# Kernel tuning notes

Measured on AMD Instinct MI355X. Metric: run time of the kernel, lower is better.

## Reference

```python
import jax, jax.numpy as jnp
import numpy as np

B, N_IN, N_OUT, H = 64, 5023, 5023, 256
EPS = 1e-12  # matches torch F.normalize default eps


def setup_inputs() -> dict:
    key = jax.random.key(0)
    k1, k2, k3, k4 = jax.random.split(key, 4)
    return {
        "x": jax.random.normal(k1, (B, N_IN, 3), dtype=jnp.float32),
        "key_w": jax.random.normal(k2, (N_IN, H), dtype=jnp.float32) * (1.0 / np.sqrt(H)),
        "query_w": jax.random.normal(k3, (H, N_OUT), dtype=jnp.float32) * (1.0 / np.sqrt(H)),
        "value_w": jax.random.normal(k4, (3, 3), dtype=jnp.float32),
    }


def reference(x, key_w, query_w, value_w):
    # v = nn.Linear(3,3,bias=False)(x): x @ W^T        [B, N_in, 3]
    v = jnp.einsum("bnd,ed->bne", x, value_w)
    # score = (key @ query) / sqrt(hidden_dim)          [N_in, N_out]
    scale = jnp.asarray(key_w.shape[-1], x.dtype) ** 0.5
    score = jnp.matmul(key_w, query_w) / scale
    # L1 normalization along dim=1 (F.normalize p=1)
    l1 = jnp.sum(jnp.abs(score), axis=1, keepdims=True)
    score = score / jnp.maximum(l1, EPS)
    # y = score.T @ v (dropout is identity in eval / p=0) [B, N_out, 3]
    return jnp.einsum("io,bid->bod", score, v)
```

## Files before the change

### kernel.cpp

```cpp
#include <hip/hip_runtime.h>
#include <hip/hip_bf16.h>

#define N_IN   5023
#define B_SZ   64
#define H_DIM  256
#define NPAD   5120
#define NBD    192
#define SPLITZ 80
#define OUT_ELEMS (B_SZ * N_IN * 3)

typedef short bf16x8 __attribute__((ext_vector_type(8)));
typedef float f32x4  __attribute__((ext_vector_type(4)));
typedef int   i32x4  __attribute__((ext_vector_type(4)));
typedef int   i32x8  __attribute__((ext_vector_type(8)));

__device__ inline void async_copy16(const void* g, void* l) {
    __builtin_amdgcn_global_load_lds(
        (const __attribute__((address_space(1))) unsigned int*)g,
        (__attribute__((address_space(3))) unsigned int*)l,
        16, 0, 0);
}

__device__ inline unsigned char to_fp8(float v) {
    int p = __builtin_amdgcn_cvt_pk_fp8_f32(v, 0.0f, 0, false);
    return (unsigned char)(p & 0xFF);
}

__global__ void conv_all(const float* __restrict__ kw, const float* __restrict__ qw,
                         unsigned char* __restrict__ k8, short* __restrict__ keyT,
                         unsigned char* __restrict__ q8, short* __restrict__ qtb,
                         float* __restrict__ l1) {
    __shared__ float tile[32][33];
    const int hb = blockIdx.x * 32;
    const int nb = blockIdx.y * 32;
    const int tx = threadIdx.x;
    const int ty = threadIdx.y;
    if (blockIdx.z == 0) {
        for (int j = 0; j < 32; j += 8) {
            int i = nb + ty + j;
            int h = hb + tx;
            float v = (i < N_IN) ? kw[(size_t)i * H_DIM + h] : 0.0f;
            tile[ty + j][tx] = v;
            k8[(size_t)i * H_DIM + h] = to_fp8(v);
        }
        __syncthreads();
        __hip_bfloat16* kt = (__hip_bfloat16*)keyT;
        for (int j = 0; j < 32; j += 8) {
            int h = hb + ty + j;
            int i = nb + tx;
            kt[(size_t)h * NPAD + i] = __float2bfloat16(tile[tx][ty + j]);
        }
        if (blockIdx.x == 0 && ty == 0) l1[nb + tx] = 0.0f;
    } else {
        for (int j = 0; j < 32; j += 8) {
            int h = hb + ty + j;
            int o = nb + tx;
            tile[ty + j][tx] = (o < N_IN) ? qw[(size_t)h * N_IN + o] : 0.0f;
        }
        __syncthreads();
        __hip_bfloat16* qt = (__hip_bfloat16*)qtb;
        for (int j = 0; j < 32; j += 8) {
            int o = nb + ty + j;
            int h = hb + tx;
            float v = tile[tx][ty + j];
            qt[(size_t)o * H_DIM + h] = __float2bfloat16(v * 0.0625f);
            q8[(size_t)o * H_DIM + h] = to_fp8(v);
        }
    }
}

__launch_bounds__(256)
__global__ void gemm_l1(const unsigned char* __restrict__ q8,
                        const unsigned char* __restrict__ k8,
                        float* __restrict__ l1) {
    __shared__ unsigned char As8[128 * 128];
    __shared__ unsigned char Bs8[128 * 128];
    const int bm = blockIdx.x, bn = blockIdx.y;
    const int tid = threadIdx.x, lane = tid & 63, wid = tid >> 6;
    const int wave_m = wid >> 1, wave_n = wid & 1;
    const int r = lane >> 3;
    const int s = lane & 7;
    const int quad = lane >> 4, cit = lane & 15;
    const int xk = cit & 7;

    f32x4 acc[4][4];
    const f32x4 zf = {0.f, 0.f, 0.f, 0.f};
    for (int a = 0; a < 4; ++a)
        for (int b = 0; b < 4; ++b) acc[a][b] = zf;

    const int g0 = (2 * quad) ^ xk;
    const int g1 = (2 * quad + 1) ^ xk;

    for (int kb = 0; kb < H_DIM; kb += 128) {
        __syncthreads();
        const int koff = kb + ((s ^ r) << 4);
        for (int c = 0; c < 4; ++c) {
            int q = wid * 4 + c;
            int row = q * 8 + r;
            async_copy16(q8 + (size_t)(bm * 128 + row) * H_DIM + koff, As8 + q * 1024);
            async_copy16(k8 + (size_t)(bn * 128 + row) * H_DIM + koff, Bs8 + q * 1024);
        }
        __syncthreads();
        i32x8 af[4];
        for (int t = 0; t < 4; ++t) {
            const unsigned char* pa = As8 + (wave_m * 64 + t * 16 + cit) * 128;
            i32x4 lo = *(const i32x4*)(pa + (g0 << 4));
            i32x4 hi = *(const i32x4*)(pa + (g1 << 4));
            af[t] = __builtin_shufflevector(lo, hi, 0, 1, 2, 3, 4, 5, 6, 7);
        }
        for (int tn = 0; tn < 4; ++tn) {
            const unsigned char* pb = Bs8 + (wave_n * 64 + tn * 16 + cit) * 128;
            i32x4 lo = *(const i32x4*)(pb + (g0 << 4));
            i32x4 hi = *(const i32x4*)(pb + (g1 << 4));
            i32x8 bf = __builtin_shufflevector(lo, hi, 0, 1, 2, 3, 4, 5, 6, 7);
            for (int tm = 0; tm < 4; ++tm)
                acc[tm][tn] = __builtin_amdgcn_mfma_scale_f32_16x16x128_f8f6f4(
                    af[tm], bf, acc[tm][tn], 0, 0,
                    0, 0x7F7F7F7F,
                    0, 0x7F7F7F7F);
        }
    }

    for (int tn = 0; tn < 4; ++tn) {
        int ig = bn * 128 + wave_n * 64 + tn * 16 + cit;
        float p = 0.0f;
        for (int tm = 0; tm < 4; ++tm) {
            f32x4 c = acc[tm][tn];
            p += fabsf(c.x) + fabsf(c.y) + fabsf(c.z) + fabsf(c.w);
        }
        p += __shfl_xor(p, 16);
        p += __shfl_xor(p, 32);
        if (quad == 0) atomicAdd(&l1[ig], p);
    }
}

#define AP 72
__launch_bounds__(256)
__global__ void gemm3_f(const float* __restrict__ x, const float* __restrict__ vw,
                        const float* __restrict__ l1, const short* __restrict__ keyT,
                        float* __restrict__ part2) {
    __shared__ short As[NBD * AP];
    __shared__ short Bs[64 * 64];
    const int bh = blockIdx.x;
    const int z  = blockIdx.y;
    const int tid = threadIdx.x, lane = tid & 63, wid = tid >> 6;
    const int wave_m = wid >> 1, wave_n = wid & 1;
    const int rr = lane >> 3, ss = lane & 7;
    const int quad = lane >> 4, cit = lane & 15;

    {
        const int i_loc = tid & 63;
        const int grp   = tid >> 6;
        const int i = z * 64 + i_loc;
        const bool ok = (i < N_IN);
        float rcp = 0.0f;
        if (ok) rcp = 1.0f / fmaxf(l1[i] * 0.0625f, 1e-12f);
        float w00 = vw[0], w01 = vw[1], w02 = vw[2];
        float w10 = vw[3], w11 = vw[4], w12 = vw[5];
        float w20 = vw[6], w21 = vw[7], w22 = vw[8];
        __hip_bfloat16* as = (__hip_bfloat16*)As;
        for (int bo = 0; bo < 16; ++bo) {
            int b = grp * 16 + bo;
            float x0 = 0.f, x1 = 0.f, x2 = 0.f;
            if (ok) {
                const float* xp = x + ((size_t)b * N_IN + i) * 3;
                x0 = xp[0]; x1 = xp[1]; x2 = xp[2];
            }
            as[(b * 3 + 0) * AP + i_loc] = __float2bfloat16((x0 * w00 + x1 * w01 + x2 * w02) * rcp);
            as[(b * 3 + 1) * AP + i_loc] = __float2bfloat16((x0 * w10 + x1 * w11 + x2 * w12) * rcp);
            as[(b * 3 + 2) * AP + i_loc] = __float2bfloat16((x0 * w20 + x1 * w21 + x2 * w22) * rcp);
        }
    }
    for (int c = 0; c < 2; ++c) {
        int q = wid * 2 + c;
        int row = q * 8 + rr;
        int koff = z * 64 + ((ss ^ (rr & 7)) << 3);
        async_copy16(keyT + (size_t)(bh * 64 + row) * NPAD + koff, Bs + q * 512);
    }
    __syncthreads();

    f32x4 acc[6][2];
    const f32x4 zf = {0.f, 0.f, 0.f, 0.f};
    for (int a = 0; a < 6; ++a)
        for (int b = 0; b < 2; ++b) acc[a][b] = zf;

    for (int kk = 0; kk < 64; kk += 32) {
        bf16x8 af[6], bf[2];
        int g = (kk >> 3) + quad;
        for (int t = 0; t < 6; ++t) {
            int row = wave_m * 96 + t * 16 + cit;
            af[t] = *(const bf16x8*)(As + row * AP + kk + quad * 8);
        }
        for (int t = 0; t < 2; ++t) {
            int row = wave_n * 32 + t * 16 + cit;
            bf[t] = *(const bf16x8*)(Bs + row * 64 + ((g ^ (cit & 7)) << 3));
        }
        for (int tm = 0; tm < 6; ++tm)
            for (int tn = 0; tn < 2; ++tn)
                acc[tm][tn] = __builtin_amdgcn_mfma_f32_16x16x32_bf16(
                    af[tm], bf[tn], acc[tm][tn], 0, 0, 0);
    }

    float* pz = part2 + (size_t)z * (NBD * H_DIM);
    for (int tn = 0; tn < 2; ++tn) {
        int h = bh * 64 + wave_n * 32 + tn * 16 + cit;
        for (int tm = 0; tm < 6; ++tm) {
            int bd0 = wave_m * 96 + tm * 16 + quad * 4;
            f32x4 c = acc[tm][tn];
            for (int r2 = 0; r2 < 4; ++r2)
                pz[(size_t)(bd0 + r2) * H_DIM + h] = c[r2];
        }
    }
}

__global__ void reduce_T(const float* __restrict__ part2, short* __restrict__ T) {
    int idx = blockIdx.x * 256 + threadIdx.x;
    float s = 0.0f;
    for (int z = 0; z < SPLITZ; ++z)
        s += part2[(size_t)z * (NBD * H_DIM) + idx];
    ((__hip_bfloat16*)T)[idx] = __float2bfloat16(s);
}

#define CS_PITCH 196
__launch_bounds__(256)
__global__ void gemm4(const short* __restrict__ qt, const short* __restrict__ T,
                      float* __restrict__ out) {
    __shared__ __align__(16) char smem[28672];
    short* As = (short*)smem;
    short* Bs = (short*)(smem + 4096);
    const int bm = blockIdx.x;
    const int tid = threadIdx.x, lane = tid & 63, wid = tid >> 6;
    const int wave_m = wid >> 1, wave_n = wid & 1;
    const int rr = lane >> 3, ss = lane & 7;
    const int quad = lane >> 4, cit = lane & 15;

    f32x4 acc[6];
    const f32x4 zf = {0.f, 0.f, 0.f, 0.f};
    for (int b = 0; b < 6; ++b) acc[b] = zf;

    for (int kb = 0; kb < H_DIM; kb += 64) {
        __syncthreads();
        const int koff = kb + ((ss ^ (rr & 7)) << 3);
        {
            int row = wid * 8 + rr;
            async_copy16(qt + (size_t)(bm * 32 + row) * H_DIM + koff, As + wid * 512);
        }
        for (int c = 0; c < 6; ++c) {
            int q = wid * 6 + c;
            int row = q * 8 + rr;
            async_copy16(T + (size_t)row * H_DIM + koff, Bs + q * 512);
        }
        __syncthreads();
        for (int kk = 0; kk < 64; kk += 32) {
            bf16x8 af, bf[6];
            int g = (kk >> 3) + quad;
            int slot = (g ^ (cit & 7)) << 3;
            {
                int row = wave_m * 16 + cit;
                af = *(const bf16x8*)(As + row * 64 + slot);
            }
            for (int t = 0; t < 6; ++t) {
                int row = wave_n * 96 + t * 16 + cit;
                bf[t] = *(const bf16x8*)(Bs + row * 64 + slot);
            }
            for (int tn = 0; tn < 6; ++tn)
                acc[tn] = __builtin_amdgcn_mfma_f32_16x16x32_bf16(
                    af, bf[tn], acc[tn], 0, 0, 0);
        }
    }

    __syncthreads();
    float* cs = (float*)smem;
    for (int tn = 0; tn < 6; ++tn) {
        int bd = wave_n * 96 + tn * 16 + cit;
        int o0 = wave_m * 16 + quad * 4;
        f32x4 c = acc[tn];
        for (int r2 = 0; r2 < 4; ++r2)
            cs[(o0 + r2) * CS_PITCH + bd] = c[r2];
    }
    __syncthreads();
    for (int it = 0; it < 24; ++it) {
        int flat = it * 256 + tid;
        int b = flat / 96;
        int w = flat - b * 96;
        int o_l = w / 3, d = w - o_l * 3;
        int og = bm * 32 + o_l;
        if (og < N_IN)
            out[(size_t)b * (N_IN * 3) + (size_t)og * 3 + d] =
                cs[o_l * CS_PITCH + b * 3 + d];
    }
}

extern "C" void kernel_launch(void* const* d_in, const int* in_sizes, int n_in,
                              void* d_out, int out_size, void* d_ws, size_t ws_size,
                              hipStream_t stream) {
    const float* x  = (const float*)d_in[0];
    const float* kw = (const float*)d_in[1];
    const float* qw = (const float*)d_in[2];
    const float* vw = (const float*)d_in[3];
    float* out = (float*)d_out;

    char* w = (char*)d_ws;
    short* qtb  = (short*)(w + 0);
    short* keyT = (short*)(w + 2621440);
    unsigned char* q8 = (unsigned char*)(w + 5242880);
    unsigned char* k8 = (unsigned char*)(w + 6553600);
    float* l1    = (float*)(w + 7864320);
    float* part2 = (float*)(w + 7884800);
    short* T     = (short*)(w + 23613440);

    conv_all<<<dim3(H_DIM / 32, NPAD / 32, 2), dim3(32, 8), 0, stream>>>(
        kw, qw, k8, keyT, q8, qtb, l1);
    gemm_l1<<<dim3(NPAD / 128, NPAD / 128), 256, 0, stream>>>(q8, k8, l1);
    gemm3_f<<<dim3(H_DIM / 64, SPLITZ), 256, 0, stream>>>(x, vw, l1, keyT, part2);
    reduce_T<<<(NBD * H_DIM) / 256, 256, 0, stream>>>(part2, T);
    gemm4<<<NPAD / 32, 256, 0, stream>>>(qtb, T, out);
}
```

Baseline: 106.5 us.

## Fuse tail GEMMs and reduction into one cooperative kernel with grid syncs

Merges gemm3_f, reduce_T and gemm4 into a single cooperative kernel of 320 blocks, using grid.sync() between phases in place of separate kernel launches. gemm_l1 now loads both K halves into double-sized shared buffers up front and needs only one barrier instead of per-iteration syncs. The aim is to remove launch gaps and tail effects. In exchange, grid-wide barriers add cost, the kernel requires cooperative launch residency, and gemm_l1 now uses 64KB of shared memory, which may lower occupancy.

```diff
diff --git a/kernel.cpp b/kernel.cpp
--- a/kernel.cpp
+++ b/kernel.cpp
@@ -1,5 +1,8 @@
 #include <hip/hip_runtime.h>
 #include <hip/hip_bf16.h>
+#include <hip/hip_cooperative_groups.h>
+
+namespace cg = cooperative_groups;
 
 #define N_IN   5023
 #define B_SZ   64
@@ -73,8 +76,8 @@
 __global__ void gemm_l1(const unsigned char* __restrict__ q8,
                         const unsigned char* __restrict__ k8,
                         float* __restrict__ l1) {
-    __shared__ unsigned char As8[128 * 128];
-    __shared__ unsigned char Bs8[128 * 128];
+    __shared__ unsigned char As8[2][128 * 128];
+    __shared__ unsigned char Bs8[2][128 * 128];
     const int bm = blockIdx.x, bn = blockIdx.y;
     const int tid = threadIdx.x, lane = tid & 63, wid = tid >> 6;
     const int wave_m = wid >> 1, wave_n = wid & 1;
@@ -83,6 +86,16 @@
     const int quad = lane >> 4, cit = lane & 15;
     const int xk = cit & 7;
 
+    for (int hf = 0; hf < 2; ++hf) {
+        const int koff = hf * 128 + ((s ^ r) << 4);
+        for (int c = 0; c < 4; ++c) {
+            int q = wid * 4 + c;
+            int row = q * 8 + r;
+            async_copy16(q8 + (size_t)(bm * 128 + row) * H_DIM + koff, As8[hf] + q * 1024);
+            async_copy16(k8 + (size_t)(bn * 128 + row) * H_DIM + koff, Bs8[hf] + q * 1024);
+        }
+    }
+
     f32x4 acc[4][4];
     const f32x4 zf = {0.f, 0.f, 0.f, 0.f};
     for (int a = 0; a < 4; ++a)
@@ -91,25 +104,18 @@
     const int g0 = (2 * quad) ^ xk;
     const int g1 = (2 * quad + 1) ^ xk;
 
-    for (int kb = 0; kb < H_DIM; kb += 128) {
-        __syncthreads();
-        const int koff = kb + ((s ^ r) << 4);
-        for (int c = 0; c < 4; ++c) {
-            int q = wid * 4 + c;
-            int row = q * 8 + r;
-            async_copy16(q8 + (size_t)(bm * 128 + row) * H_DIM + koff, As8 + q * 1024);
-            async_copy16(k8 + (size_t)(bn * 128 + row) * H_DIM + koff, Bs8 + q * 1024);
-        }
-        __syncthreads();
+    __syncthreads();
+
+    for (int hf = 0; hf < 2; ++hf) {
         i32x8 af[4];
         for (int t = 0; t < 4; ++t) {
-            const unsigned char* pa = As8 + (wave_m * 64 + t * 16 + cit) * 128;
+            const unsigned char* pa = As8[hf] + (wave_m * 64 + t * 16 + cit) * 128;
             i32x4 lo = *(const i32x4*)(pa + (g0 << 4));
             i32x4 hi = *(const i32x4*)(pa + (g1 << 4));
             af[t] = __builtin_shufflevector(lo, hi, 0, 1, 2, 3, 4, 5, 6, 7);
         }
         for (int tn = 0; tn < 4; ++tn) {
-            const unsigned char* pb = Bs8 + (wave_n * 64 + tn * 16 + cit) * 128;
+            const unsigned char* pb = Bs8[hf] + (wave_n * 64 + tn * 16 + cit) * 128;
             i32x4 lo = *(const i32x4*)(pb + (g0 << 4));
             i32x4 hi = *(const i32x4*)(pb + (g1 << 4));
             i32x8 bf = __builtin_shufflevector(lo, hi, 0, 1, 2, 3, 4, 5, 6, 7);
@@ -135,159 +141,166 @@
 }
 
 #define AP 72
-__launch_bounds__(256)
-__global__ void gemm3_f(const float* __restrict__ x, const float* __restrict__ vw,
-                        const float* __restrict__ l1, const short* __restrict__ keyT,
-                        float* __restrict__ part2) {
-    __shared__ short As[NBD * AP];
-    __shared__ short Bs[64 * 64];
-    const int bh = blockIdx.x;
-    const int z  = blockIdx.y;
+#define CS_PITCH 196
+__launch_bounds__(256, 2)
+__global__ void fused_tail(const float* __restrict__ x, const float* __restrict__ vw,
+                           const float* __restrict__ l1, const short* __restrict__ keyT,
+                           float* __restrict__ part2, short* __restrict__ T,
+                           const short* __restrict__ qt, float* __restrict__ out) {
+    __shared__ __align__(16) char smem[36864];
+    cg::grid_group grid = cg::this_grid();
+
+    const int bid = blockIdx.x;
     const int tid = threadIdx.x, lane = tid & 63, wid = tid >> 6;
     const int wave_m = wid >> 1, wave_n = wid & 1;
     const int rr = lane >> 3, ss = lane & 7;
     const int quad = lane >> 4, cit = lane & 15;
 
     {
-        const int i_loc = tid & 63;
-        const int grp   = tid >> 6;
-        const int i = z * 64 + i_loc;
-        const bool ok = (i < N_IN);
-        float rcp = 0.0f;
-        if (ok) rcp = 1.0f / fmaxf(l1[i] * 0.0625f, 1e-12f);
-        float w00 = vw[0], w01 = vw[1], w02 = vw[2];
-        float w10 = vw[3], w11 = vw[4], w12 = vw[5];
-        float w20 = vw[6], w21 = vw[7], w22 = vw[8];
-        __hip_bfloat16* as = (__hip_bfloat16*)As;
-        for (int bo = 0; bo < 16; ++bo) {
-            int b = grp * 16 + bo;
-            float x0 = 0.f, x1 = 0.f, x2 = 0.f;
-            if (ok) {
-                const float* xp = x + ((size_t)b * N_IN + i) * 3;
-                x0 = xp[0]; x1 = xp[1]; x2 = xp[2];
-            }
-            as[(b * 3 + 0) * AP + i_loc] = __float2bfloat16((x0 * w00 + x1 * w01 + x2 * w02) * rcp);
-            as[(b * 3 + 1) * AP + i_loc] = __float2bfloat16((x0 * w10 + x1 * w11 + x2 * w12) * rcp);
-            as[(b * 3 + 2) * AP + i_loc] = __float2bfloat16((x0 * w20 + x1 * w21 + x2 * w22) * rcp);
-        }
-    }
-    for (int c = 0; c < 2; ++c) {
-        int q = wid * 2 + c;
-        int row = q * 8 + rr;
-        int koff = z * 64 + ((ss ^ (rr & 7)) << 3);
-        async_copy16(keyT + (size_t)(bh * 64 + row) * NPAD + koff, Bs + q * 512);
-    }
-    __syncthreads();
-
-    f32x4 acc[6][2];
-    const f32x4 zf = {0.f, 0.f, 0.f, 0.f};
-    for (int a = 0; a < 6; ++a)
-        for (int b = 0; b < 2; ++b) acc[a][b] = zf;
-
-    for (int kk = 0; kk < 64; kk += 32) {
-        bf16x8 af[6], bf[2];
-        int g = (kk >> 3) + quad;
-        for (int t = 0; t < 6; ++t) {
-            int row = wave_m * 96 + t * 16 + cit;
-            af[t] = *(const bf16x8*)(As + row * AP + kk + quad * 8);
-        }
-        for (int t = 0; t < 2; ++t) {
-            int row = wave_n * 32 + t * 16 + cit;
-            bf[t] = *(const bf16x8*)(Bs + row * 64 + ((g ^ (cit & 7)) << 3));
-        }
-        for (int tm = 0; tm < 6; ++tm)
-            for (int tn = 0; tn < 2; ++tn)
-                acc[tm][tn] = __builtin_amdgcn_mfma_f32_16x16x32_bf16(
-                    af[tm], bf[tn], acc[tm][tn], 0, 0, 0);
-    }
-
-    float* pz = part2 + (size_t)z * (NBD * H_DIM);
-    for (int tn = 0; tn < 2; ++tn) {
-        int h = bh * 64 + wave_n * 32 + tn * 16 + cit;
-        for (int tm = 0; tm < 6; ++tm) {
-            int bd0 = wave_m * 96 + tm * 16 + quad * 4;
-            f32x4 c = acc[tm][tn];
+        short* As = (short*)smem;
+        short* Bs = (short*)(smem + 27648);
+        const int bh = bid & 3;
+        const int z  = bid >> 2;
+
+        {
+            const int i_loc = tid & 63;
+            const int grp   = tid >> 6;
+            const int i = z * 64 + i_loc;
+            const bool ok = (i < N_IN);
+            float rcp = 0.0f;
+            if (ok) rcp = 1.0f / fmaxf(l1[i] * 0.0625f, 1e-12f);
+            float w00 = vw[0], w01 = vw[1], w02 = vw[2];
+            float w10 = vw[3], w11 = vw[4], w12 = vw[5];
+            float w20 = vw[6], w21 = vw[7], w22 = vw[8];
+            __hip_bfloat16* as = (__hip_bfloat16*)As;
+            for (int bo = 0; bo < 16; ++bo) {
+                int b = grp * 16 + bo;
+                float x0 = 0.f, x1 = 0.f, x2 = 0.f;
+                if (ok) {
+                    const float* xp = x + ((size_t)b * N_IN + i) * 3;
+                    x0 = xp[0]; x1 = xp[1]; x2 = xp[2];
+                }
+                as[(b * 3 + 0) * AP + i_loc] = __float2bfloat16((x0 * w00 + x1 * w01 + x2 * w02) * rcp);
+                as[(b * 3 + 1) * AP + i_loc] = __float2bfloat16((x0 * w10 + x1 * w11 + x2 * w12) * rcp);
+                as[(b * 3 + 2) * AP + i_loc] = __float2bfloat16((x0 * w20 + x1 * w21 + x2 * w22) * rcp);
+            }
+        }
+        for (int c = 0; c < 2; ++c) {
+            int q = wid * 2 + c;
+            int row = q * 8 + rr;
+            int koff = z * 64 + ((ss ^ (rr & 7)) << 3);
+            async_copy16(keyT + (size_t)(bh * 64 + row) * NPAD + koff, Bs + q * 512);
+        }
+        __syncthreads();
+
+        f32x4 acc[6][2];
+        const f32x4 zf = {0.f, 0.f, 0.f, 0.f};
+        for (int a = 0; a < 6; ++a)
+            for (int b = 0; b < 2; ++b) acc[a][b] = zf;
+
+        for (int kk = 0; kk < 64; kk += 32) {
+            bf16x8 af[6], bf[2];
+            int g = (kk >> 3) + quad;
+            for (int t = 0; t < 6; ++t) {
+                int row = wave_m * 96 + t * 16 + cit;
+                af[t] = *(const bf16x8*)(As + row * AP + kk + quad * 8);
+            }
+            for (int t = 0; t < 2; ++t) {
+                int row = wave_n * 32 + t * 16 + cit;
+                bf[t] = *(const bf16x8*)(Bs + row * 64 + ((g ^ (cit & 7)) << 3));
+            }
+            for (int tm = 0; tm < 6; ++tm)
+                for (int tn = 0; tn < 2; ++tn)
+                    acc[tm][tn] = __builtin_amdgcn_mfma_f32_16x16x32_bf16(
+                        af[tm], bf[tn], acc[tm][tn], 0, 0, 0);
+        }
+
+        float* pz = part2 + (size_t)z * (NBD * H_DIM);
+        for (int tn = 0; tn < 2; ++tn) {
+            int h = bh * 64 + wave_n * 32 + tn * 16 + cit;
+            for (int tm = 0; tm < 6; ++tm) {
+                int bd0 = wave_m * 96 + tm * 16 + quad * 4;
+                f32x4 c = acc[tm][tn];
+                for (int r2 = 0; r2 < 4; ++r2)
+                    pz[(size_t)(bd0 + r2) * H_DIM + h] = c[r2];
+            }
+        }
+    }
+
+    grid.sync();
+
+    {
+        int idx = bid * 256 + tid;
+        if (idx < NBD * H_DIM) {
+            float sum = 0.0f;
+            for (int z = 0; z < SPLITZ; ++z)
+                sum += part2[(size_t)z * (NBD * H_DIM) + idx];
+            ((__hip_bfloat16*)T)[idx] = __float2bfloat16(sum);
+        }
+    }
+
+    grid.sync();
+
+    if (bid < NPAD / 32) {
+        short* As = (short*)smem;
+        short* Bs = (short*)(smem + 4096);
+        const int bm = bid;
+
+        f32x4 acc[6];
+        const f32x4 zf = {0.f, 0.f, 0.f, 0.f};
+        for (int b = 0; b < 6; ++b) acc[b] = zf;
+
+        for (int kb = 0; kb < H_DIM; kb += 64) {
+            __syncthreads();
+            const int koff = kb + ((ss ^ (rr & 7)) << 3);
+            {
+                int row = wid * 8 + rr;
+                async_copy16(qt + (size_t)(bm * 32 + row) * H_DIM + koff, As + wid * 512);
+            }
+            for (int c = 0; c < 6; ++c) {
+                int q = wid * 6 + c;
+                int row = q * 8 + rr;
+                async_copy16(T + (size_t)row * H_DIM + koff, Bs + q * 512);
+            }
+            __syncthreads();
+            for (int kk = 0; kk < 64; kk += 32) {
+                bf16x8 af, bf[6];
+                int g = (kk >> 3) + quad;
+                int slot = (g ^ (cit & 7)) << 3;
+                {
+                    int row = wave_m * 16 + cit;
+                    af = *(const bf16x8*)(As + row * 64 + slot);
+                }
+                for (int t = 0; t < 6; ++t) {
+                    int row = wave_n * 96 + t * 16 + cit;
+                    bf[t] = *(const bf16x8*)(Bs + row * 64 + slot);
+                }
+                for (int tn = 0; tn < 6; ++tn)
+                    acc[tn] = __builtin_amdgcn_mfma_f32_16x16x32_bf16(
+                        af, bf[tn], acc[tn], 0, 0, 0);
+            }
+        }
+
+        __syncthreads();
+        float* cs = (float*)smem;
+        for (int tn = 0; tn < 6; ++tn) {
+            int bd = wave_n * 96 + tn * 16 + cit;
+            int o0 = wave_m * 16 + quad * 4;
+            f32x4 c = acc[tn];
             for (int r2 = 0; r2 < 4; ++r2)
-                pz[(size_t)(bd0 + r2) * H_DIM + h] = c[r2];
-        }
-    }
-}
-
-__global__ void reduce_T(const float* __restrict__ part2, short* __restrict__ T) {
-    int idx = blockIdx.x * 256 + threadIdx.x;
-    float s = 0.0f;
-    for (int z = 0; z < SPLITZ; ++z)
-        s += part2[(size_t)z * (NBD * H_DIM) + idx];
-    ((__hip_bfloat16*)T)[idx] = __float2bfloat16(s);
-}
-
-#define CS_PITCH 196
-__launch_bounds__(256)
-__global__ void gemm4(const short* __restrict__ qt, const short* __restrict__ T,
-                      float* __restrict__ out) {
-    __shared__ __align__(16) char smem[28672];
-    short* As = (short*)smem;
-    short* Bs = (short*)(smem + 4096);
-    const int bm = blockIdx.x;
-    const int tid = threadIdx.x, lane = tid & 63, wid = tid >> 6;
-    const int wave_m = wid >> 1, wave_n = wid & 1;
-    const int rr = lane >> 3, ss = lane & 7;
-    const int quad = lane >> 4, cit = lane & 15;
-
-    f32x4 acc[6];
-    const f32x4 zf = {0.f, 0.f, 0.f, 0.f};
-    for (int b = 0; b < 6; ++b) acc[b] = zf;
-
-    for (int kb = 0; kb < H_DIM; kb += 64) {
-        __syncthreads();
-        const int koff = kb + ((ss ^ (rr & 7)) << 3);
-        {
-            int row = wid * 8 + rr;
-            async_copy16(qt + (size_t)(bm * 32 + row) * H_DIM + koff, As + wid * 512);
-        }
-        for (int c = 0; c < 6; ++c) {
-            int q = wid * 6 + c;
-            int row = q * 8 + rr;
-            async_copy16(T + (size_t)row * H_DIM + koff, Bs + q * 512);
-        }
-        __syncthreads();
-        for (int kk = 0; kk < 64; kk += 32) {
-            bf16x8 af, bf[6];
-            int g = (kk >> 3) + quad;
-            int slot = (g ^ (cit & 7)) << 3;
-            {
-                int row = wave_m * 16 + cit;
-                af = *(const bf16x8*)(As + row * 64 + slot);
-            }
-            for (int t = 0; t < 6; ++t) {
-                int row = wave_n * 96 + t * 16 + cit;
-                bf[t] = *(const bf16x8*)(Bs + row * 64 + slot);
-            }
-            for (int tn = 0; tn < 6; ++tn)
-                acc[tn] = __builtin_amdgcn_mfma_f32_16x16x32_bf16(
-                    af, bf[tn], acc[tn], 0, 0, 0);
-        }
-    }
-
-    __syncthreads();
-    float* cs = (float*)smem;
-    for (int tn = 0; tn < 6; ++tn) {
-        int bd = wave_n * 96 + tn * 16 + cit;
-        int o0 = wave_m * 16 + quad * 4;
-        f32x4 c = acc[tn];
-        for (int r2 = 0; r2 < 4; ++r2)
-            cs[(o0 + r2) * CS_PITCH + bd] = c[r2];
-    }
-    __syncthreads();
-    for (int it = 0; it < 24; ++it) {
-        int flat = it * 256 + tid;
-        int b = flat / 96;
-        int w = flat - b * 96;
-        int o_l = w / 3, d = w - o_l * 3;
-        int og = bm * 32 + o_l;
-        if (og < N_IN)
-            out[(size_t)b * (N_IN * 3) + (size_t)og * 3 + d] =
-                cs[o_l * CS_PITCH + b * 3 + d];
+                cs[(o0 + r2) * CS_PITCH + bd] = c[r2];
+        }
+        __syncthreads();
+        for (int it = 0; it < 24; ++it) {
+            int flat = it * 256 + tid;
+            int b = flat / 96;
+            int w = flat - b * 96;
+            int o_l = w / 3, d = w - o_l * 3;
+            int og = bm * 32 + o_l;
+            if (og < N_IN)
+                out[(size_t)b * (N_IN * 3) + (size_t)og * 3 + d] =
+                    cs[o_l * CS_PITCH + b * 3 + d];
+        }
     }
 }
 
@@ -312,7 +325,9 @@
     conv_all<<<dim3(H_DIM / 32, NPAD / 32, 2), dim3(32, 8), 0, stream>>>(
         kw, qw, k8, keyT, q8, qtb, l1);
     gemm_l1<<<dim3(NPAD / 128, NPAD / 128), 256, 0, stream>>>(q8, k8, l1);
-    gemm3_f<<<dim3(H_DIM / 64, SPLITZ), 256, 0, stream>>>(x, vw, l1, keyT, part2);
-    reduce_T<<<(NBD * H_DIM) / 256, 256, 0, stream>>>(part2, T);
-    gemm4<<<NPAD / 32, 256, 0, stream>>>(qtb, T, out);
-}
+
+    void* args[] = {(void*)&x, (void*)&vw, (void*)&l1, (void*)&keyT,
+                    (void*)&part2, (void*)&T, (void*)&qtb, (void*)&out};
+    hipLaunchCooperativeKernel((void*)fused_tail, dim3(SPLITZ * 4), dim3(256),
+                               args, 0, stream);
+}
```

Result: slower. 203.7 us (+91.3%).
